# Performance work log

Measured on AMD Instinct MI355X. Metric: run time of the kernel, lower is better.

Reference implementation:

```python
import jax, jax.numpy as jnp
import numpy as np

N_NODES = 20000
N_EDGES = 320000
N_GRAPHS = 64
IN_DIM = 39
HID = 128
HEADS = 4
NUM_CONV = 3
PRED_HID = 32
N_TASKS = 1
NEG_SLOPE = 0.2


def setup_inputs() -> dict:
    key = jax.random.key(0)
    ks = jax.random.split(key, 16)
    node_feat = jax.random.normal(ks[0], (N_NODES, IN_DIM), dtype=jnp.float32)
    edge_index = jax.random.randint(ks[1], (2, N_EDGES), 0, N_NODES, dtype=jnp.int64)
    batch = jnp.sort(jax.random.randint(ks[2], (N_NODES,), 0, N_GRAPHS, dtype=jnp.int64))
    s = 0.05
    return {
        "node_feat": node_feat,
        "edge_index": edge_index,
        "batch": batch,
        "emb_W": jax.random.normal(ks[3], (IN_DIM, HID), dtype=jnp.float32) * s,
        "emb_b": jnp.zeros((HID,), dtype=jnp.float32),
        "lin_W": jax.random.normal(ks[4], (NUM_CONV, HID, HEADS * HID), dtype=jnp.float32) * s,
        "att_src": jax.random.normal(ks[5], (NUM_CONV, HEADS, HID), dtype=jnp.float32) * s,
        "att_dst": jax.random.normal(ks[6], (NUM_CONV, HEADS, HID), dtype=jnp.float32) * s,
        "conv_b": jnp.zeros((NUM_CONV, HID), dtype=jnp.float32),
        "fc_W": jax.random.normal(ks[7], (HID, PRED_HID), dtype=jnp.float32) * s,
        "fc_b": jnp.zeros((PRED_HID,), dtype=jnp.float32),
        "out_W": jax.random.normal(ks[8], (PRED_HID, N_TASKS), dtype=jnp.float32) * s,
        "out_b": jnp.zeros((N_TASKS,), dtype=jnp.float32),
    }


def _gat_layer(x, src, dst, W, a_src, a_dst, b):
    # PyG GATConv (concat=False): per-head projection, additive attention,
    # segment softmax over incoming edges of each target node, head-mean + bias.
    N = x.shape[0]
    h = (x @ W).reshape(N, HEADS, HID)            # [N, H, F]
    a_s = jnp.einsum('nhf,hf->nh', h, a_src)       # [N, H]
    a_d = jnp.einsum('nhf,hf->nh', h, a_dst)       # [N, H]
    e = jax.nn.leaky_relu(a_s[src] + a_d[dst], NEG_SLOPE)   # [E, H]
    e_max = jax.ops.segment_max(e, dst, num_segments=N)      # [N, H]
    e = jnp.exp(e - e_max[dst])
    denom = jax.ops.segment_sum(e, dst, num_segments=N)      # [N, H]
    alpha = e / denom[dst]                                    # [E, H]
    msg = h[src] * alpha[..., None]                           # [E, H, F]
    out = jax.ops.segment_sum(msg, dst, num_segments=N)      # [N, H, F]
    return out.mean(axis=1) + b                               # [N, F]


def reference(node_feat, edge_index, batch, emb_W, emb_b, lin_W, att_src, att_dst,
              conv_b, fc_W, fc_b, out_W, out_b):
    N = node_feat.shape[0]
    loops = jnp.arange(N, dtype=edge_index.dtype)
    src = jnp.concatenate([edge_index[0], loops])  # add_self_loops=True
    dst = jnp.concatenate([edge_index[1], loops])

    x = node_feat @ emb_W + emb_b
    for l in range(NUM_CONV):
        x = _gat_layer(x, src, dst, lin_W[l], att_src[l], att_dst[l], conv_b[l])

    # global_mean_pool
    sums = jax.ops.segment_sum(x, batch, num_segments=N_GRAPHS)              # [G, F]
    cnt = jax.ops.segment_sum(jnp.ones((N,), x.dtype), batch, num_segments=N_GRAPHS)
    g = sums / jnp.maximum(cnt, 1.0)[:, None]

    g = g @ fc_W + fc_b
    return g @ out_W + out_b
```

## Files before the change

### kernel.cpp

```cpp
#include <hip/hip_runtime.h>
#include <math.h>

#define N_NODES 20000
#define E0      320000
#define E_TOT   (E0 + N_NODES)
#define N_GRAPHS 64
#define IN_DIM  39
#define HID     128
#define HEADS   4
#define HHID    (HEADS * HID)
#define NUM_CONV 3
#define PRED_HID 32
#define NEG_SLOPE 0.2f

__device__ __forceinline__ int esrc(const int* __restrict__ ei, int e) {
    return e < E0 ? ei[e] : (e - E0);
}
__device__ __forceinline__ int edst(const int* __restrict__ ei, int e) {
    return e < E0 ? ei[E0 + e] : (e - E0);
}

__global__ void k_deg(const int* __restrict__ ei, int* __restrict__ deg) {
    int e = blockIdx.x * blockDim.x + threadIdx.x;
    if (e >= E_TOT) return;
    atomicAdd(&deg[edst(ei, e)], 1);
}

__global__ __launch_bounds__(1024) void k_scan(const int* __restrict__ deg,
                                               int* __restrict__ row_ptr,
                                               int* __restrict__ cursor) {
    __shared__ int part[1024];
    const int CHUNK = 20;
    int t = threadIdx.x;
    int base = t * CHUNK;
    int s = 0;
    for (int i = 0; i < CHUNK; i++) {
        int idx = base + i;
        if (idx < N_NODES) s += deg[idx];
    }
    part[t] = s;
    __syncthreads();
    for (int off = 1; off < 1024; off <<= 1) {
        int v = (t >= off) ? part[t - off] : 0;
        __syncthreads();
        part[t] += v;
        __syncthreads();
    }
    int run = part[t] - s;
    for (int i = 0; i < CHUNK; i++) {
        int idx = base + i;
        if (idx < N_NODES) {
            row_ptr[idx] = run;
            cursor[idx]  = run;
            run += deg[idx];
        }
    }
    if (t == 1023) row_ptr[N_NODES] = part[1023];
}

__global__ void k_scatter(const int* __restrict__ ei, int* __restrict__ cursor,
                          int* __restrict__ csr_src) {
    int e = blockIdx.x * blockDim.x + threadIdx.x;
    if (e >= E_TOT) return;
    int d = edst(ei, e);
    int pos = atomicAdd(&cursor[d], 1);
    csr_src[pos] = esrc(ei, e);
}

__global__ __launch_bounds__(128) void k_emb(const float* __restrict__ nf,
                                             const float* __restrict__ W,
                                             const float* __restrict__ b,
                                             float* __restrict__ x) {
    __shared__ float f[IN_DIM];
    int n = blockIdx.x, t = threadIdx.x;
    if (t < IN_DIM) f[t] = nf[(size_t)n * IN_DIM + t];
    __syncthreads();
    float acc = b[t];
#pragma unroll
    for (int k = 0; k < IN_DIM; k++) acc += f[k] * W[k * HID + t];
    x[(size_t)n * HID + t] = acc;
}

__global__ __launch_bounds__(128) void k_wsd(const float* __restrict__ lin_W,
                                             const float* __restrict__ attS,
                                             const float* __restrict__ attD,
                                             float* __restrict__ Wsd) {
    int l = blockIdx.x >> 3, j = blockIdx.x & 7, k = threadIdx.x;
    int h = j & 3;
    const float* Wl = lin_W + (size_t)l * HID * HHID;
    const float* av = ((j < 4) ? attS : attD) + ((size_t)l * HEADS + h) * HID;
    const float* wr = Wl + (size_t)k * HHID + h * HID;
    float dot = 0.f;
#pragma unroll 4
    for (int f = 0; f < HID; f++) dot += wr[f] * av[f];
    Wsd[(size_t)l * 8 * HID + j * HID + k] = dot;
}

__global__ __launch_bounds__(256) void k_attproj(const float* __restrict__ x,
                                                 const float* __restrict__ WsdL,
                                                 float* __restrict__ A8) {
    __shared__ float sW[8 * HID];
    for (int i = threadIdx.x; i < 8 * HID; i += 256) sW[i] = WsdL[i];
    __syncthreads();
    int wid = threadIdx.x >> 6, lane = threadIdx.x & 63;
    int n = blockIdx.x * 4 + wid;
    if (n >= N_NODES) return;
    float2 xv = *(const float2*)(x + (size_t)n * HID + lane * 2);
    float p[8];
#pragma unroll
    for (int j = 0; j < 8; j++) {
        float v = xv.x * sW[j * HID + lane * 2] + xv.y * sW[j * HID + lane * 2 + 1];
#pragma unroll
        for (int off = 32; off; off >>= 1) v += __shfl_xor(v, off, 64);
        p[j] = v;
    }
    if (lane == 0) {
        *(float4*)(A8 + (size_t)n * 8)     = make_float4(p[0], p[1], p[2], p[3]);
        *(float4*)(A8 + (size_t)n * 8 + 4) = make_float4(p[4], p[5], p[6], p[7]);
    }
}

__global__ __launch_bounds__(256) void k_aggr(const float* __restrict__ x,
                                              const int* __restrict__ row_ptr,
                                              const int* __restrict__ csr_src,
                                              const float* __restrict__ A8,
                                              float* __restrict__ agg) {
    int wid = threadIdx.x >> 6, lane = threadIdx.x & 63;
    int n = blockIdx.x * 4 + wid;
    if (n >= N_NODES) return;
    float4 vd = *(const float4*)(A8 + (size_t)n * 8 + 4);
    int beg = row_ptr[n], end = row_ptr[n + 1];
    float a0x = 0.f, a0y = 0.f, a1x = 0.f, a1y = 0.f;
    float a2x = 0.f, a2y = 0.f, a3x = 0.f, a3y = 0.f;
    float d0 = 0.f, d1 = 0.f, d2 = 0.f, d3 = 0.f;
    size_t lo = (size_t)(lane * 2);
    int eu = lane >> 2, eh = lane & 3;
    float vdh = (eh == 0) ? vd.x : (eh == 1) ? vd.y : (eh == 2) ? vd.z : vd.w;
    int i = beg;
    for (; i + 4 <= end; i += 4) {
        int s0 = csr_src[i];
        int s1 = csr_src[i + 1];
        int s2 = csr_src[i + 2];
        int s3 = csr_src[i + 3];
        float e = 0.f;
        if (lane < 16) {
            int su = (eu == 0) ? s0 : (eu == 1) ? s1 : (eu == 2) ? s2 : s3;
            float v = A8[(size_t)su * 8 + eh] + vdh;
            v = fmaxf(v, NEG_SLOPE * v);
            e = __expf(v);
        }
        float2 xv0 = *(const float2*)(x + (size_t)s0 * HID + lo);
        float2 xv1 = *(const float2*)(x + (size_t)s1 * HID + lo);
        float2 xv2 = *(const float2*)(x + (size_t)s2 * HID + lo);
        float2 xv3 = *(const float2*)(x + (size_t)s3 * HID + lo);
        float e00 = __shfl(e, 0, 64),  e01 = __shfl(e, 1, 64),  e02 = __shfl(e, 2, 64),  e03 = __shfl(e, 3, 64);
        float e10 = __shfl(e, 4, 64),  e11 = __shfl(e, 5, 64),  e12 = __shfl(e, 6, 64),  e13 = __shfl(e, 7, 64);
        float e20 = __shfl(e, 8, 64),  e21 = __shfl(e, 9, 64),  e22 = __shfl(e, 10, 64), e23 = __shfl(e, 11, 64);
        float e30 = __shfl(e, 12, 64), e31 = __shfl(e, 13, 64), e32 = __shfl(e, 14, 64), e33 = __shfl(e, 15, 64);
        a0x += e00 * xv0.x; a0y += e00 * xv0.y;
        a1x += e01 * xv0.x; a1y += e01 * xv0.y;
        a2x += e02 * xv0.x; a2y += e02 * xv0.y;
        a3x += e03 * xv0.x; a3y += e03 * xv0.y;
        d0 += e00; d1 += e01; d2 += e02; d3 += e03;
        a0x += e10 * xv1.x; a0y += e10 * xv1.y;
        a1x += e11 * xv1.x; a1y += e11 * xv1.y;
        a2x += e12 * xv1.x; a2y += e12 * xv1.y;
        a3x += e13 * xv1.x; a3y += e13 * xv1.y;
        d0 += e10; d1 += e11; d2 += e12; d3 += e13;
        a0x += e20 * xv2.x; a0y += e20 * xv2.y;
        a1x += e21 * xv2.x; a1y += e21 * xv2.y;
        a2x += e22 * xv2.x; a2y += e22 * xv2.y;
        a3x += e23 * xv2.x; a3y += e23 * xv2.y;
        d0 += e20; d1 += e21; d2 += e22; d3 += e23;
        a0x += e30 * xv3.x; a0y += e30 * xv3.y;
        a1x += e31 * xv3.x; a1y += e31 * xv3.y;
        a2x += e32 * xv3.x; a2y += e32 * xv3.y;
        a3x += e33 * xv3.x; a3y += e33 * xv3.y;
        d0 += e30; d1 += e31; d2 += e32; d3 += e33;
    }
    for (; i < end; i++) {
        int s0 = csr_src[i];
        float4 vs = *(const float4*)(A8 + (size_t)s0 * 8);
        float2 xv0 = *(const float2*)(x + (size_t)s0 * HID + lo);
        float v0 = vs.x + vd.x; v0 = fmaxf(v0, NEG_SLOPE * v0); float e0 = __expf(v0);
        float v1 = vs.y + vd.y; v1 = fmaxf(v1, NEG_SLOPE * v1); float e1 = __expf(v1);
        float v2 = vs.z + vd.z; v2 = fmaxf(v2, NEG_SLOPE * v2); float e2 = __expf(v2);
        float v3 = vs.w + vd.w; v3 = fmaxf(v3, NEG_SLOPE * v3); float e3 = __expf(v3);
        a0x += e0 * xv0.x; a0y += e0 * xv0.y;
        a1x += e1 * xv0.x; a1y += e1 * xv0.y;
        a2x += e2 * xv0.x; a2y += e2 * xv0.y;
        a3x += e3 * xv0.x; a3y += e3 * xv0.y;
        d0 += e0; d1 += e1; d2 += e2; d3 += e3;
    }
    float i0 = 1.f / d0, i1 = 1.f / d1, i2 = 1.f / d2, i3 = 1.f / d3;
    float* ag = agg + (size_t)n * HHID;
    *(float2*)(ag + 0 * HID + lo) = make_float2(a0x * i0, a0y * i0);
    *(float2*)(ag + 1 * HID + lo) = make_float2(a1x * i1, a1y * i1);
    *(float2*)(ag + 2 * HID + lo) = make_float2(a2x * i2, a2y * i2);
    *(float2*)(ag + 3 * HID + lo) = make_float2(a3x * i3, a3y * i3);
}

#define G2_BM 64
#define G2_KSPLIT 4
__global__ __launch_bounds__(256) void k_gemm2(const float* __restrict__ agg,
                                               const float* __restrict__ W,
                                               float* __restrict__ part, int M) {
    __shared__ float At[64][G2_BM];
    __shared__ float Bs[64][HID];
    int tid = threadIdx.x;
    int row0 = blockIdx.x * G2_BM;
    int ks = blockIdx.y;
    int ty = tid >> 4, tx = tid & 15;
    int r0 = ty * 4, c0 = tx * 4;
    float acc[4][8] = {};

#pragma unroll
    for (int kt = 0; kt < 2; kt++) {
        int kbase = ks * 128 + kt * 64;
        __syncthreads();
#pragma unroll
        for (int i = 0; i < 4; i++) {
            int idx = tid + i * 256;
            int r = idx >> 4;
            int c4 = idx & 15;
            int gr = row0 + r;
            float4 v = make_float4(0.f, 0.f, 0.f, 0.f);
            if (gr < M) v = *(const float4*)(agg + (size_t)gr * HHID + kbase + c4 * 4);
            int sw = (((r >> 2) ^ c4) << 2) + (r & 3);
            At[c4 * 4 + 0][sw] = v.x;
            At[c4 * 4 + 1][sw] = v.y;
            At[c4 * 4 + 2][sw] = v.z;
            At[c4 * 4 + 3][sw] = v.w;
        }
#pragma unroll
        for (int i = 0; i < 8; i++) {
            int idx = tid + i * 256;
            int kr = idx >> 5;
            int c4 = idx & 31;
            int kg = kbase + kr;
            int hd = kg >> 7, kk = kg & 127;
            *(float4*)(&Bs[kr][c4 * 4]) =
                *(const float4*)(W + (size_t)kk * HHID + hd * HID + c4 * 4);
        }
        __syncthreads();
#pragma unroll 4
        for (int k = 0; k < 64; k++) {
            float4 av = *(float4*)(&At[k][((ty ^ (k >> 2)) << 2)]);
            float4 b1 = *(float4*)(&Bs[k][c0]);
            float4 b2 = *(float4*)(&Bs[k][c0 + 64]);
            acc[0][0] += av.x * b1.x; acc[0][1] += av.x * b1.y; acc[0][2] += av.x * b1.z; acc[0][3] += av.x * b1.w;
            acc[0][4] += av.x * b2.x; acc[0][5] += av.x * b2.y; acc[0][6] += av.x * b2.z; acc[0][7] += av.x * b2.w;
            acc[1][0] += av.y * b1.x; acc[1][1] += av.y * b1.y; acc[1][2] += av.y * b1.z; acc[1][3] += av.y * b1.w;
            acc[1][4] += av.y * b2.x; acc[1][5] += av.y * b2.y; acc[1][6] += av.y * b2.z; acc[1][7] += av.y * b2.w;
            acc[2][0] += av.z * b1.x; acc[2][1] += av.z * b1.y; acc[2][2] += av.z * b1.z; acc[2][3] += av.z * b1.w;
            acc[2][4] += av.z * b2.x; acc[2][5] += av.z * b2.y; acc[2][6] += av.z * b2.z; acc[2][7] += av.z * b2.w;
            acc[3][0] += av.w * b1.x; acc[3][1] += av.w * b1.y; acc[3][2] += av.w * b1.z; acc[3][3] += av.w * b1.w;
            acc[3][4] += av.w * b2.x; acc[3][5] += av.w * b2.y; acc[3][6] += av.w * b2.z; acc[3][7] += av.w * b2.w;
        }
    }
    float* pb = part + (size_t)ks * M * HID;
#pragma unroll
    for (int i = 0; i < 4; i++) {
        int gr = row0 + r0 + i;
        if (gr < M) {
            *(float4*)(pb + (size_t)gr * HID + c0) =
                make_float4(acc[i][0], acc[i][1], acc[i][2], acc[i][3]);
            *(float4*)(pb + (size_t)gr * HID + c0 + 64) =
                make_float4(acc[i][4], acc[i][5], acc[i][6], acc[i][7]);
        }
    }
}

__global__ __launch_bounds__(256) void k_gfin(const float* __restrict__ part,
                                              const float* __restrict__ bias,
                                              const float* __restrict__ WsdL,
                                              float* __restrict__ xn,
                                              float* __restrict__ A8, int M) {
    __shared__ float sW[8 * HID];
    for (int i = threadIdx.x; i < 8 * HID; i += 256) sW[i] = WsdL[i];
    __syncthreads();
    int wid = threadIdx.x >> 6, lane = threadIdx.x & 63;
    int n = blockIdx.x * 4 + wid;
    if (n >= M) return;
    size_t off = (size_t)n * HID + lane * 2;
    size_t str = (size_t)M * HID;
    float2 p0 = *(const float2*)(part + off);
    float2 p1 = *(const float2*)(part + str + off);
    float2 p2 = *(const float2*)(part + 2 * str + off);
    float2 p3 = *(const float2*)(part + 3 * str + off);
    float2 bb = *(const float2*)(bias + lane * 2);
    float2 xv;
    xv.x = 0.25f * (p0.x + p1.x + p2.x + p3.x) + bb.x;
    xv.y = 0.25f * (p0.y + p1.y + p2.y + p3.y) + bb.y;
    *(float2*)(xn + off) = xv;
    float p[8];
#pragma unroll
    for (int j = 0; j < 8; j++) {
        float v = xv.x * sW[j * HID + lane * 2] + xv.y * sW[j * HID + lane * 2 + 1];
#pragma unroll
        for (int o = 32; o; o >>= 1) v += __shfl_xor(v, o, 64);
        p[j] = v;
    }
    if (lane == 0) {
        *(float4*)(A8 + (size_t)n * 8)     = make_float4(p[0], p[1], p[2], p[3]);
        *(float4*)(A8 + (size_t)n * 8 + 4) = make_float4(p[4], p[5], p[6], p[7]);
    }
}

#define POOL_NPB 64
__global__ __launch_bounds__(128) void k_pool(const float* __restrict__ x,
                                              const int* __restrict__ batch,
                                              float* __restrict__ g_sum,
                                              int* __restrict__ g_cnt) {
    int t = threadIdx.x;
    int n0 = blockIdx.x * POOL_NPB;
    int n1 = n0 + POOL_NPB; if (n1 > N_NODES) n1 = N_NODES;
    if (n0 >= n1) return;
    int cur = batch[n0];
    float acc = 0.f;
    int cnt = 0;
    for (int n = n0; n < n1; n++) {
        int b = batch[n];
        if (b != cur) {
            atomicAdd(&g_sum[cur * HID + t], acc);
            if (t == 0) atomicAdd(&g_cnt[cur], cnt);
            acc = 0.f; cnt = 0; cur = b;
        }
        acc += x[(size_t)n * HID + t];
        cnt++;
    }
    atomicAdd(&g_sum[cur * HID + t], acc);
    if (t == 0) atomicAdd(&g_cnt[cur], cnt);
}

__global__ __launch_bounds__(64) void k_head(const float* __restrict__ g_sum,
                                             const int* __restrict__ g_cnt,
                                             const float* __restrict__ fcW,
                                             const float* __restrict__ fcb,
                                             const float* __restrict__ outW,
                                             const float* __restrict__ outb,
                                             float* __restrict__ out) {
    int g = blockIdx.x, t = threadIdx.x;
    float inv = 1.f / fmaxf((float)g_cnt[g], 1.f);
    float val = 0.f;
    if (t < PRED_HID) {
        float dot = fcb[t];
        for (int f = 0; f < HID; f++)
            dot += (g_sum[g * HID + f] * inv) * fcW[f * PRED_HID + t];
        val = dot * outW[t];
    }
#pragma unroll
    for (int off = 32; off; off >>= 1) val += __shfl_xor(val, off, 64);
    if (t == 0) out[g] = val + outb[0];
}

extern "C" void kernel_launch(void* const* d_in, const int* in_sizes, int n_in,
                              void* d_out, int out_size, void* d_ws, size_t ws_size,
                              hipStream_t stream) {
    const float* node_feat = (const float*)d_in[0];
    const int*   edge_index = (const int*)d_in[1];
    const int*   batch     = (const int*)d_in[2];
    const float* emb_W     = (const float*)d_in[3];
    const float* emb_b     = (const float*)d_in[4];
    const float* lin_W     = (const float*)d_in[5];
    const float* att_src   = (const float*)d_in[6];
    const float* att_dst   = (const float*)d_in[7];
    const float* conv_b    = (const float*)d_in[8];
    const float* fc_W      = (const float*)d_in[9];
    const float* fc_b      = (const float*)d_in[10];
    const float* out_W     = (const float*)d_in[11];
    const float* out_b     = (const float*)d_in[12];
    float* out = (float*)d_out;

    char* p = (char*)d_ws;
    auto alloc = [&](size_t bytes) {
        void* r = (void*)p;
        p += (bytes + 255) & ~(size_t)255;
        return r;
    };
    float* x0      = (float*)alloc((size_t)N_NODES * HID * 4);
    float* x1      = (float*)alloc((size_t)N_NODES * HID * 4);
    float* agg     = (float*)alloc((size_t)N_NODES * HHID * 4);
    float* part    = (float*)alloc((size_t)G2_KSPLIT * N_NODES * HID * 4);
    float* A8      = (float*)alloc((size_t)N_NODES * 8 * 4);
    float* Wsd     = (float*)alloc((size_t)NUM_CONV * 8 * HID * 4);
    int*   deg     = (int*)alloc((size_t)(N_NODES + 1) * 4);
    int*   row_ptr = (int*)alloc((size_t)(N_NODES + 1) * 4);
    int*   cursor  = (int*)alloc((size_t)N_NODES * 4);
    int*   csr_src = (int*)alloc((size_t)E_TOT * 4);
    float* g_sum   = (float*)alloc((size_t)N_GRAPHS * HID * 4);
    int*   g_cnt   = (int*)alloc((size_t)N_GRAPHS * 4);

    const int EB = (E_TOT + 255) / 256;
    const int NB4 = (N_NODES + 3) / 4;

    hipMemsetAsync(deg, 0, (size_t)N_NODES * 4, stream);
    k_deg<<<EB, 256, 0, stream>>>(edge_index, deg);
    k_scan<<<1, 1024, 0, stream>>>(deg, row_ptr, cursor);
    k_scatter<<<EB, 256, 0, stream>>>(edge_index, cursor, csr_src);

    k_wsd<<<NUM_CONV * 8, 128, 0, stream>>>(lin_W, att_src, att_dst, Wsd);

    k_emb<<<N_NODES, 128, 0, stream>>>(node_feat, emb_W, emb_b, x0);
    k_attproj<<<NB4, 256, 0, stream>>>(x0, Wsd, A8);

    float* xin = x0;
    float* xout = x1;
    for (int l = 0; l < NUM_CONV; l++) {
        const float* Wl = lin_W + (size_t)l * HID * HHID;
        const float* bl = conv_b + (size_t)l * HID;
        int lnext = (l + 1 < NUM_CONV) ? l + 1 : NUM_CONV - 1;

        k_aggr<<<NB4, 256, 0, stream>>>(xin, row_ptr, csr_src, A8, agg);
        dim3 gg((N_NODES + G2_BM - 1) / G2_BM, G2_KSPLIT);
        k_gemm2<<<gg, 256, 0, stream>>>(agg, Wl, part, N_NODES);
        k_gfin<<<NB4, 256, 0, stream>>>(part, bl, Wsd + (size_t)lnext * 8 * HID,
                                        xout, A8, N_NODES);
        float* tmp = xin; xin = xout; xout = tmp;
    }

    hipMemsetAsync(g_sum, 0, (size_t)N_GRAPHS * HID * 4, stream);
    hipMemsetAsync(g_cnt, 0, (size_t)N_GRAPHS * 4, stream);
    k_pool<<<(N_NODES + POOL_NPB - 1) / POOL_NPB, 128, 0, stream>>>(xin, batch, g_sum, g_cnt);
    k_head<<<N_GRAPHS, 64, 0, stream>>>(g_sum, g_cnt, fc_W, fc_b,
                                        out_W, out_b, out);
}
```

Measured before the change: 410.9 us.

## Fuse whole GAT pipeline into one persistent cooperative kernel with grid syncs

Replaces the chain of separate kernel launches (CSR build, embedding, attention projection, per-layer aggregation, GEMM, finalize, pooling, head) with a single cooperative persistent kernel that separates phases using grid.sync(). The goal is to remove launch overhead and the inter-kernel gaps. The CSR scan becomes a multi-block hierarchical scan, and embedding is fused with the attention projection. In exchange, the grid is capped at the cooperative occupancy limit and every phase runs at that fixed parallelism, and the grid-wide barriers add cost. Heavy shared memory use at launch bounds of 3 blocks per CU may also limit occupancy for the gather-bound aggregation.

```diff
diff --git a/kernel.cpp b/kernel.cpp
--- a/kernel.cpp
+++ b/kernel.cpp
@@ -1,5 +1,8 @@
 #include <hip/hip_runtime.h>
+#include <hip/hip_cooperative_groups.h>
 #include <math.h>
+
+namespace cg = cooperative_groups;
 
 #define N_NODES 20000
 #define E0      320000
@@ -12,6 +15,18 @@
 #define NUM_CONV 3
 #define PRED_HID 32
 #define NEG_SLOPE 0.2f
+#define KSPLIT  4
+#define NTILES  ((N_NODES + 63) / 64)
+
+struct MegaParams {
+    const float* node_feat; const int* edge_index; const int* batch;
+    const float* emb_W; const float* emb_b; const float* lin_W;
+    const float* att_src; const float* att_dst; const float* conv_b;
+    const float* fc_W; const float* fc_b; const float* out_W; const float* out_b;
+    float* out;
+    float* x0; float* x1; float* agg; float* part; float* A8; float* Wsd;
+    int* deg; int* row_ptr; int* cursor; int* csr_src; int* bsum; int* bpre;
+};
 
 __device__ __forceinline__ int esrc(const int* __restrict__ ei, int e) {
     return e < E0 ? ei[e] : (e - E0);
@@ -19,409 +34,373 @@
 __device__ __forceinline__ int edst(const int* __restrict__ ei, int e) {
     return e < E0 ? ei[E0 + e] : (e - E0);
 }
-
-__global__ void k_deg(const int* __restrict__ ei, int* __restrict__ deg) {
-    int e = blockIdx.x * blockDim.x + threadIdx.x;
-    if (e >= E_TOT) return;
-    atomicAdd(&deg[edst(ei, e)], 1);
+__device__ __forceinline__ int lbound(const int* __restrict__ a, int n, int v) {
+    int lo = 0, hi = n;
+    while (lo < hi) { int m = (lo + hi) >> 1; if (a[m] < v) lo = m + 1; else hi = m; }
+    return lo;
 }
 
-__global__ __launch_bounds__(1024) void k_scan(const int* __restrict__ deg,
-                                               int* __restrict__ row_ptr,
-                                               int* __restrict__ cursor) {
-    __shared__ int part[1024];
-    const int CHUNK = 20;
-    int t = threadIdx.x;
-    int base = t * CHUNK;
-    int s = 0;
-    for (int i = 0; i < CHUNK; i++) {
-        int idx = base + i;
-        if (idx < N_NODES) s += deg[idx];
-    }
-    part[t] = s;
-    __syncthreads();
-    for (int off = 1; off < 1024; off <<= 1) {
-        int v = (t >= off) ? part[t - off] : 0;
+__global__ __launch_bounds__(256, 3) void k_mega(MegaParams P) {
+    cg::grid_group grid = cg::this_grid();
+    const int G = gridDim.x, b = blockIdx.x, tid = threadIdx.x;
+    const int gthread = b * 256 + tid, nthreads = G * 256;
+    const int wid = tid >> 6, lane = tid & 63;
+
+    __shared__ __align__(16) char smem_raw[49152];
+    int*   ib  = (int*)smem_raw;
+    float* fsh = (float*)smem_raw;
+    float* At  = (float*)smem_raw;
+    float* Bs  = (float*)(smem_raw + 16384);
+
+    for (int i = gthread; i < N_NODES; i += nthreads) P.deg[i] = 0;
+    for (int u = b; u < NUM_CONV * 8; u += G) {
+        int l = u >> 3, j = u & 7, h = j & 3;
+        if (tid < HID) {
+            const float* wr = P.lin_W + (size_t)l * HID * HHID + (size_t)tid * HHID + h * HID;
+            const float* av = ((j < 4) ? P.att_src : P.att_dst) + ((size_t)l * HEADS + h) * HID;
+            float dot = 0.f;
+            for (int f = 0; f < HID; f++) dot += wr[f] * av[f];
+            P.Wsd[(size_t)l * 8 * HID + j * HID + tid] = dot;
+        }
+    }
+    grid.sync();
+
+    for (int e = gthread; e < E_TOT; e += nthreads)
+        atomicAdd(&P.deg[edst(P.edge_index, e)], 1);
+    grid.sync();
+
+    const int C = (N_NODES + G - 1) / G;
+    const int nlo = b * C, nhi = (nlo + C < N_NODES) ? nlo + C : N_NODES;
+    {
+        int s = 0;
+        for (int i = nlo + tid; i < nhi; i += 256) s += P.deg[i];
+        ib[tid] = s; __syncthreads();
+        for (int off = 128; off; off >>= 1) { if (tid < off) ib[tid] += ib[tid + off]; __syncthreads(); }
+        if (tid == 0) P.bsum[b] = ib[0];
+    }
+    grid.sync();
+
+    if (b == 0) {
+        int per = (G + 255) / 256;
+        int vals[8]; int loc = 0;
+        for (int i2 = 0; i2 < per; i2++) {
+            int idx = tid * per + i2;
+            int v = (idx < G) ? P.bsum[idx] : 0;
+            vals[i2] = v; loc += v;
+        }
+        ib[tid] = loc; __syncthreads();
+        for (int off = 1; off < 256; off <<= 1) {
+            int v = (tid >= off) ? ib[tid - off] : 0;
+            __syncthreads(); ib[tid] += v; __syncthreads();
+        }
+        int run = ib[tid] - loc;
+        for (int i2 = 0; i2 < per; i2++) {
+            int idx = tid * per + i2;
+            if (idx < G) { P.bpre[idx] = run; run += vals[i2]; }
+        }
+        if (tid == 255) P.row_ptr[N_NODES] = ib[255];
+    }
+    grid.sync();
+
+    {
+        int cnt = nhi - nlo;
+        if (tid < cnt) ib[tid] = P.deg[nlo + tid];
         __syncthreads();
-        part[t] += v;
+        if (tid == 0) {
+            int run = P.bpre[b];
+            for (int i = 0; i < cnt; i++) { int d = ib[i]; ib[i] = run; run += d; }
+        }
         __syncthreads();
-    }
-    int run = part[t] - s;
-    for (int i = 0; i < CHUNK; i++) {
-        int idx = base + i;
-        if (idx < N_NODES) {
-            row_ptr[idx] = run;
-            cursor[idx]  = run;
-            run += deg[idx];
-        }
-    }
-    if (t == 1023) row_ptr[N_NODES] = part[1023];
-}
-
-__global__ void k_scatter(const int* __restrict__ ei, int* __restrict__ cursor,
-                          int* __restrict__ csr_src) {
-    int e = blockIdx.x * blockDim.x + threadIdx.x;
-    if (e >= E_TOT) return;
-    int d = edst(ei, e);
-    int pos = atomicAdd(&cursor[d], 1);
-    csr_src[pos] = esrc(ei, e);
-}
-
-__global__ __launch_bounds__(128) void k_emb(const float* __restrict__ nf,
-                                             const float* __restrict__ W,
-                                             const float* __restrict__ b,
-                                             float* __restrict__ x) {
-    __shared__ float f[IN_DIM];
-    int n = blockIdx.x, t = threadIdx.x;
-    if (t < IN_DIM) f[t] = nf[(size_t)n * IN_DIM + t];
-    __syncthreads();
-    float acc = b[t];
-#pragma unroll
-    for (int k = 0; k < IN_DIM; k++) acc += f[k] * W[k * HID + t];
-    x[(size_t)n * HID + t] = acc;
-}
-
-__global__ __launch_bounds__(128) void k_wsd(const float* __restrict__ lin_W,
-                                             const float* __restrict__ attS,
-                                             const float* __restrict__ attD,
-                                             float* __restrict__ Wsd) {
-    int l = blockIdx.x >> 3, j = blockIdx.x & 7, k = threadIdx.x;
-    int h = j & 3;
-    const float* Wl = lin_W + (size_t)l * HID * HHID;
-    const float* av = ((j < 4) ? attS : attD) + ((size_t)l * HEADS + h) * HID;
-    const float* wr = Wl + (size_t)k * HHID + h * HID;
-    float dot = 0.f;
+        if (tid < cnt) { P.row_ptr[nlo + tid] = ib[tid]; P.cursor[nlo + tid] = ib[tid]; }
+    }
+    grid.sync();
+
+    for (int e = gthread; e < E_TOT; e += nthreads) {
+        int d = edst(P.edge_index, e);
+        int pos = atomicAdd(&P.cursor[d], 1);
+        P.csr_src[pos] = esrc(P.edge_index, e);
+    }
+    for (int grp = b; grp < N_NODES / 4; grp += G) {
+        int n = grp * 4 + wid;
+        if (lane < IN_DIM) fsh[wid * 40 + lane] = P.node_feat[(size_t)n * IN_DIM + lane];
+        __syncthreads();
+        float2 acc = *(const float2*)(P.emb_b + lane * 2);
+#pragma unroll
+        for (int k = 0; k < IN_DIM; k++) {
+            float f = fsh[wid * 40 + k];
+            float2 w = *(const float2*)(P.emb_W + k * HID + lane * 2);
+            acc.x += f * w.x; acc.y += f * w.y;
+        }
+        *(float2*)(P.x0 + (size_t)n * HID + lane * 2) = acc;
+        float p[8];
+#pragma unroll
+        for (int j = 0; j < 8; j++) {
+            float2 w = *(const float2*)(P.Wsd + j * HID + lane * 2);
+            float v = acc.x * w.x + acc.y * w.y;
+#pragma unroll
+            for (int off = 32; off; off >>= 1) v += __shfl_xor(v, off, 64);
+            p[j] = v;
+        }
+        if (lane == 0) {
+            *(float4*)(P.A8 + (size_t)n * 8)     = make_float4(p[0], p[1], p[2], p[3]);
+            *(float4*)(P.A8 + (size_t)n * 8 + 4) = make_float4(p[4], p[5], p[6], p[7]);
+        }
+        __syncthreads();
+    }
+    grid.sync();
+
+    float* xin = P.x0;
+    float* xout = P.x1;
+    for (int l = 0; l < NUM_CONV; l++) {
+        const float* Wl = P.lin_W + (size_t)l * HID * HHID;
+        const float* bl = P.conv_b + (size_t)l * HID;
+        int lnext = (l + 1 < NUM_CONV) ? l + 1 : NUM_CONV - 1;
+        const float* WsdL = P.Wsd + (size_t)lnext * 8 * HID;
+
+        for (int grp = b; grp < N_NODES / 4; grp += G) {
+            int n = grp * 4 + wid;
+            float4 vd = *(const float4*)(P.A8 + (size_t)n * 8 + 4);
+            int beg = P.row_ptr[n], end = P.row_ptr[n + 1];
+            float a0x = 0.f, a0y = 0.f, a1x = 0.f, a1y = 0.f;
+            float a2x = 0.f, a2y = 0.f, a3x = 0.f, a3y = 0.f;
+            float d0 = 0.f, d1 = 0.f, d2 = 0.f, d3 = 0.f;
+            size_t lo2 = (size_t)(lane * 2);
+            int eu = lane >> 2, eh = lane & 3;
+            float vdh = (eh == 0) ? vd.x : (eh == 1) ? vd.y : (eh == 2) ? vd.z : vd.w;
+            int i = beg;
+            for (; i + 4 <= end; i += 4) {
+                int s0 = P.csr_src[i];
+                int s1 = P.csr_src[i + 1];
+                int s2 = P.csr_src[i + 2];
+                int s3 = P.csr_src[i + 3];
+                float e = 0.f;
+                if (lane < 16) {
+                    int su = (eu == 0) ? s0 : (eu == 1) ? s1 : (eu == 2) ? s2 : s3;
+                    float v = P.A8[(size_t)su * 8 + eh] + vdh;
+                    v = fmaxf(v, NEG_SLOPE * v);
+                    e = __expf(v);
+                }
+                float2 xv0 = *(const float2*)(xin + (size_t)s0 * HID + lo2);
+                float2 xv1 = *(const float2*)(xin + (size_t)s1 * HID + lo2);
+                float2 xv2 = *(const float2*)(xin + (size_t)s2 * HID + lo2);
+                float2 xv3 = *(const float2*)(xin + (size_t)s3 * HID + lo2);
+                float e00 = __shfl(e, 0, 64),  e01 = __shfl(e, 1, 64),  e02 = __shfl(e, 2, 64),  e03 = __shfl(e, 3, 64);
+                float e10 = __shfl(e, 4, 64),  e11 = __shfl(e, 5, 64),  e12 = __shfl(e, 6, 64),  e13 = __shfl(e, 7, 64);
+                float e20 = __shfl(e, 8, 64),  e21 = __shfl(e, 9, 64),  e22 = __shfl(e, 10, 64), e23 = __shfl(e, 11, 64);
+                float e30 = __shfl(e, 12, 64), e31 = __shfl(e, 13, 64), e32 = __shfl(e, 14, 64), e33 = __shfl(e, 15, 64);
+                a0x += e00 * xv0.x; a0y += e00 * xv0.y;
+                a1x += e01 * xv0.x; a1y += e01 * xv0.y;
+                a2x += e02 * xv0.x; a2y += e02 * xv0.y;
+                a3x += e03 * xv0.x; a3y += e03 * xv0.y;
+                d0 += e00; d1 += e01; d2 += e02; d3 += e03;
+                a0x += e10 * xv1.x; a0y += e10 * xv1.y;
+                a1x += e11 * xv1.x; a1y += e11 * xv1.y;
+                a2x += e12 * xv1.x; a2y += e12 * xv1.y;
+                a3x += e13 * xv1.x; a3y += e13 * xv1.y;
+                d0 += e10; d1 += e11; d2 += e12; d3 += e13;
+                a0x += e20 * xv2.x; a0y += e20 * xv2.y;
+                a1x += e21 * xv2.x; a1y += e21 * xv2.y;
+                a2x += e22 * xv2.x; a2y += e22 * xv2.y;
+                a3x += e23 * xv2.x; a3y += e23 * xv2.y;
+                d0 += e20; d1 += e21; d2 += e22; d3 += e23;
+                a0x += e30 * xv3.x; a0y += e30 * xv3.y;
+                a1x += e31 * xv3.x; a1y += e31 * xv3.y;
+                a2x += e32 * xv3.x; a2y += e32 * xv3.y;
+                a3x += e33 * xv3.x; a3y += e33 * xv3.y;
+                d0 += e30; d1 += e31; d2 += e32; d3 += e33;
+            }
+            for (; i < end; i++) {
+                int s0 = P.csr_src[i];
+                float4 vs = *(const float4*)(P.A8 + (size_t)s0 * 8);
+                float2 xv0 = *(const float2*)(xin + (size_t)s0 * HID + lo2);
+                float v0 = vs.x + vd.x; v0 = fmaxf(v0, NEG_SLOPE * v0); float e0 = __expf(v0);
+                float v1 = vs.y + vd.y; v1 = fmaxf(v1, NEG_SLOPE * v1); float e1 = __expf(v1);
+                float v2 = vs.z + vd.z; v2 = fmaxf(v2, NEG_SLOPE * v2); float e2 = __expf(v2);
+                float v3 = vs.w + vd.w; v3 = fmaxf(v3, NEG_SLOPE * v3); float e3 = __expf(v3);
+                a0x += e0 * xv0.x; a0y += e0 * xv0.y;
+                a1x += e1 * xv0.x; a1y += e1 * xv0.y;
+                a2x += e2 * xv0.x; a2y += e2 * xv0.y;
+                a3x += e3 * xv0.x; a3y += e3 * xv0.y;
+                d0 += e0; d1 += e1; d2 += e2; d3 += e3;
+            }
+            float i0 = 1.f / d0, i1 = 1.f / d1, i2 = 1.f / d2, i3 = 1.f / d3;
+            float* ag = P.agg + (size_t)n * HHID;
+            *(float2*)(ag + 0 * HID + lo2) = make_float2(a0x * i0, a0y * i0);
+            *(float2*)(ag + 1 * HID + lo2) = make_float2(a1x * i1, a1y * i1);
+            *(float2*)(ag + 2 * HID + lo2) = make_float2(a2x * i2, a2y * i2);
+            *(float2*)(ag + 3 * HID + lo2) = make_float2(a3x * i3, a3y * i3);
+        }
+        grid.sync();
+
+        {
+            int ty = tid >> 4, tx = tid & 15;
+            int r0 = ty * 4, c0 = tx * 4;
+            for (int u = b; u < NTILES * KSPLIT; u += G) {
+                int bm = u >> 2, ks = u & 3;
+                int row0 = bm * 64;
+                float acc[4][8] = {};
+#pragma unroll
+                for (int kt = 0; kt < 2; kt++) {
+                    int kbase = ks * 128 + kt * 64;
+                    __syncthreads();
+#pragma unroll
+                    for (int i = 0; i < 4; i++) {
+                        int idx = tid + i * 256;
+                        int r = idx >> 4, c4 = idx & 15;
+                        int gr = row0 + r;
+                        float4 v = make_float4(0.f, 0.f, 0.f, 0.f);
+                        if (gr < N_NODES) v = *(const float4*)(P.agg + (size_t)gr * HHID + kbase + c4 * 4);
+                        int sw = (((r >> 2) ^ c4) << 2) + (r & 3);
+                        At[(c4 * 4 + 0) * 64 + sw] = v.x;
+                        At[(c4 * 4 + 1) * 64 + sw] = v.y;
+                        At[(c4 * 4 + 2) * 64 + sw] = v.z;
+                        At[(c4 * 4 + 3) * 64 + sw] = v.w;
+                    }
+#pragma unroll
+                    for (int i = 0; i < 8; i++) {
+                        int idx = tid + i * 256;
+                        int kr = idx >> 5, c4 = idx & 31;
+                        int kg = kbase + kr;
+                        int hd = kg >> 7, kk = kg & 127;
+                        *(float4*)(Bs + kr * 128 + c4 * 4) =
+                            *(const float4*)(Wl + (size_t)kk * HHID + hd * HID + c4 * 4);
+                    }
+                    __syncthreads();
 #pragma unroll 4
-    for (int f = 0; f < HID; f++) dot += wr[f] * av[f];
-    Wsd[(size_t)l * 8 * HID + j * HID + k] = dot;
-}
-
-__global__ __launch_bounds__(256) void k_attproj(const float* __restrict__ x,
-                                                 const float* __restrict__ WsdL,
-                                                 float* __restrict__ A8) {
-    __shared__ float sW[8 * HID];
-    for (int i = threadIdx.x; i < 8 * HID; i += 256) sW[i] = WsdL[i];
-    __syncthreads();
-    int wid = threadIdx.x >> 6, lane = threadIdx.x & 63;
-    int n = blockIdx.x * 4 + wid;
-    if (n >= N_NODES) return;
-    float2 xv = *(const float2*)(x + (size_t)n * HID + lane * 2);
-    float p[8];
-#pragma unroll
-    for (int j = 0; j < 8; j++) {
-        float v = xv.x * sW[j * HID + lane * 2] + xv.y * sW[j * HID + lane * 2 + 1];
-#pragma unroll
-        for (int off = 32; off; off >>= 1) v += __shfl_xor(v, off, 64);
-        p[j] = v;
-    }
-    if (lane == 0) {
-        *(float4*)(A8 + (size_t)n * 8)     = make_float4(p[0], p[1], p[2], p[3]);
-        *(float4*)(A8 + (size_t)n * 8 + 4) = make_float4(p[4], p[5], p[6], p[7]);
-    }
-}
-
-__global__ __launch_bounds__(256) void k_aggr(const float* __restrict__ x,
-                                              const int* __restrict__ row_ptr,
-                                              const int* __restrict__ csr_src,
-                                              const float* __restrict__ A8,
-                                              float* __restrict__ agg) {
-    int wid = threadIdx.x >> 6, lane = threadIdx.x & 63;
-    int n = blockIdx.x * 4 + wid;
-    if (n >= N_NODES) return;
-    float4 vd = *(const float4*)(A8 + (size_t)n * 8 + 4);
-    int beg = row_ptr[n], end = row_ptr[n + 1];
-    float a0x = 0.f, a0y = 0.f, a1x = 0.f, a1y = 0.f;
-    float a2x = 0.f, a2y = 0.f, a3x = 0.f, a3y = 0.f;
-    float d0 = 0.f, d1 = 0.f, d2 = 0.f, d3 = 0.f;
-    size_t lo = (size_t)(lane * 2);
-    int eu = lane >> 2, eh = lane & 3;
-    float vdh = (eh == 0) ? vd.x : (eh == 1) ? vd.y : (eh == 2) ? vd.z : vd.w;
-    int i = beg;
-    for (; i + 4 <= end; i += 4) {
-        int s0 = csr_src[i];
-        int s1 = csr_src[i + 1];
-        int s2 = csr_src[i + 2];
-        int s3 = csr_src[i + 3];
-        float e = 0.f;
-        if (lane < 16) {
-            int su = (eu == 0) ? s0 : (eu == 1) ? s1 : (eu == 2) ? s2 : s3;
-            float v = A8[(size_t)su * 8 + eh] + vdh;
-            v = fmaxf(v, NEG_SLOPE * v);
-            e = __expf(v);
-        }
-        float2 xv0 = *(const float2*)(x + (size_t)s0 * HID + lo);
-        float2 xv1 = *(const float2*)(x + (size_t)s1 * HID + lo);
-        float2 xv2 = *(const float2*)(x + (size_t)s2 * HID + lo);
-        float2 xv3 = *(const float2*)(x + (size_t)s3 * HID + lo);
-        float e00 = __shfl(e, 0, 64),  e01 = __shfl(e, 1, 64),  e02 = __shfl(e, 2, 64),  e03 = __shfl(e, 3, 64);
-        float e10 = __shfl(e, 4, 64),  e11 = __shfl(e, 5, 64),  e12 = __shfl(e, 6, 64),  e13 = __shfl(e, 7, 64);
-        float e20 = __shfl(e, 8, 64),  e21 = __shfl(e, 9, 64),  e22 = __shfl(e, 10, 64), e23 = __shfl(e, 11, 64);
-        float e30 = __shfl(e, 12, 64), e31 = __shfl(e, 13, 64), e32 = __shfl(e, 14, 64), e33 = __shfl(e, 15, 64);
-        a0x += e00 * xv0.x; a0y += e00 * xv0.y;
-        a1x += e01 * xv0.x; a1y += e01 * xv0.y;
-        a2x += e02 * xv0.x; a2y += e02 * xv0.y;
-        a3x += e03 * xv0.x; a3y += e03 * xv0.y;
-        d0 += e00; d1 += e01; d2 += e02; d3 += e03;
-        a0x += e10 * xv1.x; a0y += e10 * xv1.y;
-        a1x += e11 * xv1.x; a1y += e11 * xv1.y;
-        a2x += e12 * xv1.x; a2y += e12 * xv1.y;
-        a3x += e13 * xv1.x; a3y += e13 * xv1.y;
-        d0 += e10; d1 += e11; d2 += e12; d3 += e13;
-        a0x += e20 * xv2.x; a0y += e20 * xv2.y;
-        a1x += e21 * xv2.x; a1y += e21 * xv2.y;
-        a2x += e22 * xv2.x; a2y += e22 * xv2.y;
-        a3x += e23 * xv2.x; a3y += e23 * xv2.y;
-        d0 += e20; d1 += e21; d2 += e22; d3 += e23;
-        a0x += e30 * xv3.x; a0y += e30 * xv3.y;
-        a1x += e31 * xv3.x; a1y += e31 * xv3.y;
-        a2x += e32 * xv3.x; a2y += e32 * xv3.y;
-        a3x += e33 * xv3.x; a3y += e33 * xv3.y;
-        d0 += e30; d1 += e31; d2 += e32; d3 += e33;
-    }
-    for (; i < end; i++) {
-        int s0 = csr_src[i];
-        float4 vs = *(const float4*)(A8 + (size_t)s0 * 8);
-        float2 xv0 = *(const float2*)(x + (size_t)s0 * HID + lo);
-        float v0 = vs.x + vd.x; v0 = fmaxf(v0, NEG_SLOPE * v0); float e0 = __expf(v0);
-        float v1 = vs.y + vd.y; v1 = fmaxf(v1, NEG_SLOPE * v1); float e1 = __expf(v1);
-        float v2 = vs.z + vd.z; v2 = fmaxf(v2, NEG_SLOPE * v2); float e2 = __expf(v2);
-        float v3 = vs.w + vd.w; v3 = fmaxf(v3, NEG_SLOPE * v3); float e3 = __expf(v3);
-        a0x += e0 * xv0.x; a0y += e0 * xv0.y;
-        a1x += e1 * xv0.x; a1y += e1 * xv0.y;
-        a2x += e2 * xv0.x; a2y += e2 * xv0.y;
-        a3x += e3 * xv0.x; a3y += e3 * xv0.y;
-        d0 += e0; d1 += e1; d2 += e2; d3 += e3;
-    }
-    float i0 = 1.f / d0, i1 = 1.f / d1, i2 = 1.f / d2, i3 = 1.f / d3;
-    float* ag = agg + (size_t)n * HHID;
-    *(float2*)(ag + 0 * HID + lo) = make_float2(a0x * i0, a0y * i0);
-    *(float2*)(ag + 1 * HID + lo) = make_float2(a1x * i1, a1y * i1);
-    *(float2*)(ag + 2 * HID + lo) = make_float2(a2x * i2, a2y * i2);
-    *(float2*)(ag + 3 * HID + lo) = make_float2(a3x * i3, a3y * i3);
-}
-
-#define G2_BM 64
-#define G2_KSPLIT 4
-__global__ __launch_bounds__(256) void k_gemm2(const float* __restrict__ agg,
-                                               const float* __restrict__ W,
-                                               float* __restrict__ part, int M) {
-    __shared__ float At[64][G2_BM];
-    __shared__ float Bs[64][HID];
-    int tid = threadIdx.x;
-    int row0 = blockIdx.x * G2_BM;
-    int ks = blockIdx.y;
-    int ty = tid >> 4, tx = tid & 15;
-    int r0 = ty * 4, c0 = tx * 4;
-    float acc[4][8] = {};
-
-#pragma unroll
-    for (int kt = 0; kt < 2; kt++) {
-        int kbase = ks * 128 + kt * 64;
+                    for (int k = 0; k < 64; k++) {
+                        float4 av = *(float4*)(At + k * 64 + ((ty ^ (k >> 2)) << 2));
+                        float4 b1 = *(float4*)(Bs + k * 128 + c0);
+                        float4 b2 = *(float4*)(Bs + k * 128 + c0 + 64);
+                        acc[0][0] += av.x * b1.x; acc[0][1] += av.x * b1.y; acc[0][2] += av.x * b1.z; acc[0][3] += av.x * b1.w;
+                        acc[0][4] += av.x * b2.x; acc[0][5] += av.x * b2.y; acc[0][6] += av.x * b2.z; acc[0][7] += av.x * b2.w;
+                        acc[1][0] += av.y * b1.x; acc[1][1] += av.y * b1.y; acc[1][2] += av.y * b1.z; acc[1][3] += av.y * b1.w;
+                        acc[1][4] += av.y * b2.x; acc[1][5] += av.y * b2.y; acc[1][6] += av.y * b2.z; acc[1][7] += av.y * b2.w;
+                        acc[2][0] += av.z * b1.x; acc[2][1] += av.z * b1.y; acc[2][2] += av.z * b1.z; acc[2][3] += av.z * b1.w;
+                        acc[2][4] += av.z * b2.x; acc[2][5] += av.z * b2.y; acc[2][6] += av.z * b2.z; acc[2][7] += av.z * b2.w;
+                        acc[3][0] += av.w * b1.x; acc[3][1] += av.w * b1.y; acc[3][2] += av.w * b1.z; acc[3][3] += av.w * b1.w;
+                        acc[3][4] += av.w * b2.x; acc[3][5] += av.w * b2.y; acc[3][6] += av.w * b2.z; acc[3][7] += av.w * b2.w;
+                    }
+                }
+                float* pb = P.part + (size_t)ks * N_NODES * HID;
+#pragma unroll
+                for (int i = 0; i < 4; i++) {
+                    int gr = row0 + r0 + i;
+                    if (gr < N_NODES) {
+                        *(float4*)(pb + (size_t)gr * HID + c0) =
+                            make_float4(acc[i][0], acc[i][1], acc[i][2], acc[i][3]);
+                        *(float4*)(pb + (size_t)gr * HID + c0 + 64) =
+                            make_float4(acc[i][4], acc[i][5], acc[i][6], acc[i][7]);
+                    }
+                }
+            }
+        }
+        grid.sync();
+
+        for (int grp = b; grp < N_NODES / 4; grp += G) {
+            int n = grp * 4 + wid;
+            size_t off = (size_t)n * HID + lane * 2;
+            size_t str = (size_t)N_NODES * HID;
+            float2 p0 = *(const float2*)(P.part + off);
+            float2 p1 = *(const float2*)(P.part + str + off);
+            float2 p2 = *(const float2*)(P.part + 2 * str + off);
+            float2 p3 = *(const float2*)(P.part + 3 * str + off);
+            float2 bb = *(const float2*)(bl + lane * 2);
+            float2 xv;
+            xv.x = 0.25f * (p0.x + p1.x + p2.x + p3.x) + bb.x;
+            xv.y = 0.25f * (p0.y + p1.y + p2.y + p3.y) + bb.y;
+            *(float2*)(xout + off) = xv;
+            float p[8];
+#pragma unroll
+            for (int j = 0; j < 8; j++) {
+                float2 w = *(const float2*)(WsdL + j * HID + lane * 2);
+                float v = xv.x * w.x + xv.y * w.y;
+#pragma unroll
+                for (int o = 32; o; o >>= 1) v += __shfl_xor(v, o, 64);
+                p[j] = v;
+            }
+            if (lane == 0) {
+                *(float4*)(P.A8 + (size_t)n * 8)     = make_float4(p[0], p[1], p[2], p[3]);
+                *(float4*)(P.A8 + (size_t)n * 8 + 4) = make_float4(p[4], p[5], p[6], p[7]);
+            }
+        }
+        grid.sync();
+
+        float* tmp = xin; xin = xout; xout = tmp;
+    }
+
+    if (b < N_GRAPHS) {
+        int g = b;
+        int start = lbound(P.batch, N_NODES, g);
+        int end   = lbound(P.batch, N_NODES, g + 1);
+        int t = tid & 127, half = tid >> 7;
+        float a = 0.f;
+        for (int n = start + half; n < end; n += 2) a += xin[(size_t)n * HID + t];
+        fsh[tid] = a; __syncthreads();
+        if (tid < HID) fsh[256 + tid] = (fsh[tid] + fsh[tid + 128]) / fmaxf((float)(end - start), 1.f);
         __syncthreads();
-#pragma unroll
-        for (int i = 0; i < 4; i++) {
-            int idx = tid + i * 256;
-            int r = idx >> 4;
-            int c4 = idx & 15;
-            int gr = row0 + r;
-            float4 v = make_float4(0.f, 0.f, 0.f, 0.f);
-            if (gr < M) v = *(const float4*)(agg + (size_t)gr * HHID + kbase + c4 * 4);
-            int sw = (((r >> 2) ^ c4) << 2) + (r & 3);
-            At[c4 * 4 + 0][sw] = v.x;
-            At[c4 * 4 + 1][sw] = v.y;
-            At[c4 * 4 + 2][sw] = v.z;
-            At[c4 * 4 + 3][sw] = v.w;
-        }
-#pragma unroll
-        for (int i = 0; i < 8; i++) {
-            int idx = tid + i * 256;
-            int kr = idx >> 5;
-            int c4 = idx & 31;
-            int kg = kbase + kr;
-            int hd = kg >> 7, kk = kg & 127;
-            *(float4*)(&Bs[kr][c4 * 4]) =
-                *(const float4*)(W + (size_t)kk * HHID + hd * HID + c4 * 4);
-        }
-        __syncthreads();
-#pragma unroll 4
-        for (int k = 0; k < 64; k++) {
-            float4 av = *(float4*)(&At[k][((ty ^ (k >> 2)) << 2)]);
-            float4 b1 = *(float4*)(&Bs[k][c0]);
-            float4 b2 = *(float4*)(&Bs[k][c0 + 64]);
-            acc[0][0] += av.x * b1.x; acc[0][1] += av.x * b1.y; acc[0][2] += av.x * b1.z; acc[0][3] += av.x * b1.w;
-            acc[0][4] += av.x * b2.x; acc[0][5] += av.x * b2.y; acc[0][6] += av.x * b2.z; acc[0][7] += av.x * b2.w;
-            acc[1][0] += av.y * b1.x; acc[1][1] += av.y * b1.y; acc[1][2] += av.y * b1.z; acc[1][3] += av.y * b1.w;
-            acc[1][4] += av.y * b2.x; acc[1][5] += av.y * b2.y; acc[1][6] += av.y * b2.z; acc[1][7] += av.y * b2.w;
-            acc[2][0] += av.z * b1.x; acc[2][1] += av.z * b1.y; acc[2][2] += av.z * b1.z; acc[2][3] += av.z * b1.w;
-            acc[2][4] += av.z * b2.x; acc[2][5] += av.z * b2.y; acc[2][6] += av.z * b2.z; acc[2][7] += av.z * b2.w;
-            acc[3][0] += av.w * b1.x; acc[3][1] += av.w * b1.y; acc[3][2] += av.w * b1.z; acc[3][3] += av.w * b1.w;
-            acc[3][4] += av.w * b2.x; acc[3][5] += av.w * b2.y; acc[3][6] += av.w * b2.z; acc[3][7] += av.w * b2.w;
-        }
-    }
-    float* pb = part + (size_t)ks * M * HID;
-#pragma unroll
-    for (int i = 0; i < 4; i++) {
-        int gr = row0 + r0 + i;
-        if (gr < M) {
-            *(float4*)(pb + (size_t)gr * HID + c0) =
-                make_float4(acc[i][0], acc[i][1], acc[i][2], acc[i][3]);
-            *(float4*)(pb + (size_t)gr * HID + c0 + 64) =
-                make_float4(acc[i][4], acc[i][5], acc[i][6], acc[i][7]);
-        }
-    }
-}
-
-__global__ __launch_bounds__(256) void k_gfin(const float* __restrict__ part,
-                                              const float* __restrict__ bias,
-                                              const float* __restrict__ WsdL,
-                                              float* __restrict__ xn,
-                                              float* __restrict__ A8, int M) {
-    __shared__ float sW[8 * HID];
-    for (int i = threadIdx.x; i < 8 * HID; i += 256) sW[i] = WsdL[i];
-    __syncthreads();
-    int wid = threadIdx.x >> 6, lane = threadIdx.x & 63;
-    int n = blockIdx.x * 4 + wid;
-    if (n >= M) return;
-    size_t off = (size_t)n * HID + lane * 2;
-    size_t str = (size_t)M * HID;
-    float2 p0 = *(const float2*)(part + off);
-    float2 p1 = *(const float2*)(part + str + off);
-    float2 p2 = *(const float2*)(part + 2 * str + off);
-    float2 p3 = *(const float2*)(part + 3 * str + off);
-    float2 bb = *(const float2*)(bias + lane * 2);
-    float2 xv;
-    xv.x = 0.25f * (p0.x + p1.x + p2.x + p3.x) + bb.x;
-    xv.y = 0.25f * (p0.y + p1.y + p2.y + p3.y) + bb.y;
-    *(float2*)(xn + off) = xv;
-    float p[8];
-#pragma unroll
-    for (int j = 0; j < 8; j++) {
-        float v = xv.x * sW[j * HID + lane * 2] + xv.y * sW[j * HID + lane * 2 + 1];
-#pragma unroll
-        for (int o = 32; o; o >>= 1) v += __shfl_xor(v, o, 64);
-        p[j] = v;
-    }
-    if (lane == 0) {
-        *(float4*)(A8 + (size_t)n * 8)     = make_float4(p[0], p[1], p[2], p[3]);
-        *(float4*)(A8 + (size_t)n * 8 + 4) = make_float4(p[4], p[5], p[6], p[7]);
-    }
-}
-
-#define POOL_NPB 64
-__global__ __launch_bounds__(128) void k_pool(const float* __restrict__ x,
-                                              const int* __restrict__ batch,
-                                              float* __restrict__ g_sum,
-                                              int* __restrict__ g_cnt) {
-    int t = threadIdx.x;
-    int n0 = blockIdx.x * POOL_NPB;
-    int n1 = n0 + POOL_NPB; if (n1 > N_NODES) n1 = N_NODES;
-    if (n0 >= n1) return;
-    int cur = batch[n0];
-    float acc = 0.f;
-    int cnt = 0;
-    for (int n = n0; n < n1; n++) {
-        int b = batch[n];
-        if (b != cur) {
-            atomicAdd(&g_sum[cur * HID + t], acc);
-            if (t == 0) atomicAdd(&g_cnt[cur], cnt);
-            acc = 0.f; cnt = 0; cur = b;
-        }
-        acc += x[(size_t)n * HID + t];
-        cnt++;
-    }
-    atomicAdd(&g_sum[cur * HID + t], acc);
-    if (t == 0) atomicAdd(&g_cnt[cur], cnt);
-}
-
-__global__ __launch_bounds__(64) void k_head(const float* __restrict__ g_sum,
-                                             const int* __restrict__ g_cnt,
-                                             const float* __restrict__ fcW,
-                                             const float* __restrict__ fcb,
-                                             const float* __restrict__ outW,
-                                             const float* __restrict__ outb,
-                                             float* __restrict__ out) {
-    int g = blockIdx.x, t = threadIdx.x;
-    float inv = 1.f / fmaxf((float)g_cnt[g], 1.f);
-    float val = 0.f;
-    if (t < PRED_HID) {
-        float dot = fcb[t];
-        for (int f = 0; f < HID; f++)
-            dot += (g_sum[g * HID + f] * inv) * fcW[f * PRED_HID + t];
-        val = dot * outW[t];
-    }
-#pragma unroll
-    for (int off = 32; off; off >>= 1) val += __shfl_xor(val, off, 64);
-    if (t == 0) out[g] = val + outb[0];
+        if (tid < 64) {
+            float val = 0.f;
+            if (tid < PRED_HID) {
+                float dot = P.fc_b[tid];
+                for (int f = 0; f < HID; f++) dot += fsh[256 + f] * P.fc_W[f * PRED_HID + tid];
+                val = dot * P.out_W[tid];
+            }
+#pragma unroll
+            for (int off = 16; off; off >>= 1) val += __shfl_down(val, off, 64);
+            if (tid == 0) P.out[g] = val + P.out_b[0];
+        }
+    }
 }
 
 extern "C" void kernel_launch(void* const* d_in, const int* in_sizes, int n_in,
                               void* d_out, int out_size, void* d_ws, size_t ws_size,
                               hipStream_t stream) {
-    const float* node_feat = (const float*)d_in[0];
-    const int*   edge_index = (const int*)d_in[1];
-    const int*   batch     = (const int*)d_in[2];
-    const float* emb_W     = (const float*)d_in[3];
-    const float* emb_b     = (const float*)d_in[4];
-    const float* lin_W     = (const float*)d_in[5];
-    const float* att_src   = (const float*)d_in[6];
-    const float* att_dst   = (const float*)d_in[7];
-    const float* conv_b    = (const float*)d_in[8];
-    const float* fc_W      = (const float*)d_in[9];
-    const float* fc_b      = (const float*)d_in[10];
-    const float* out_W     = (const float*)d_in[11];
-    const float* out_b     = (const float*)d_in[12];
-    float* out = (float*)d_out;
-
     char* p = (char*)d_ws;
     auto alloc = [&](size_t bytes) {
         void* r = (void*)p;
         p += (bytes + 255) & ~(size_t)255;
         return r;
     };
-    float* x0      = (float*)alloc((size_t)N_NODES * HID * 4);
-    float* x1      = (float*)alloc((size_t)N_NODES * HID * 4);
-    float* agg     = (float*)alloc((size_t)N_NODES * HHID * 4);
-    float* part    = (float*)alloc((size_t)G2_KSPLIT * N_NODES * HID * 4);
-    float* A8      = (float*)alloc((size_t)N_NODES * 8 * 4);
-    float* Wsd     = (float*)alloc((size_t)NUM_CONV * 8 * HID * 4);
-    int*   deg     = (int*)alloc((size_t)(N_NODES + 1) * 4);
-    int*   row_ptr = (int*)alloc((size_t)(N_NODES + 1) * 4);
-    int*   cursor  = (int*)alloc((size_t)N_NODES * 4);
-    int*   csr_src = (int*)alloc((size_t)E_TOT * 4);
-    float* g_sum   = (float*)alloc((size_t)N_GRAPHS * HID * 4);
-    int*   g_cnt   = (int*)alloc((size_t)N_GRAPHS * 4);
-
-    const int EB = (E_TOT + 255) / 256;
-    const int NB4 = (N_NODES + 3) / 4;
-
-    hipMemsetAsync(deg, 0, (size_t)N_NODES * 4, stream);
-    k_deg<<<EB, 256, 0, stream>>>(edge_index, deg);
-    k_scan<<<1, 1024, 0, stream>>>(deg, row_ptr, cursor);
-    k_scatter<<<EB, 256, 0, stream>>>(edge_index, cursor, csr_src);
-
-    k_wsd<<<NUM_CONV * 8, 128, 0, stream>>>(lin_W, att_src, att_dst, Wsd);
-
-    k_emb<<<N_NODES, 128, 0, stream>>>(node_feat, emb_W, emb_b, x0);
-    k_attproj<<<NB4, 256, 0, stream>>>(x0, Wsd, A8);
-
-    float* xin = x0;
-    float* xout = x1;
-    for (int l = 0; l < NUM_CONV; l++) {
-        const float* Wl = lin_W + (size_t)l * HID * HHID;
-        const float* bl = conv_b + (size_t)l * HID;
-        int lnext = (l + 1 < NUM_CONV) ? l + 1 : NUM_CONV - 1;
-
-        k_aggr<<<NB4, 256, 0, stream>>>(xin, row_ptr, csr_src, A8, agg);
-        dim3 gg((N_NODES + G2_BM - 1) / G2_BM, G2_KSPLIT);
-        k_gemm2<<<gg, 256, 0, stream>>>(agg, Wl, part, N_NODES);
-        k_gfin<<<NB4, 256, 0, stream>>>(part, bl, Wsd + (size_t)lnext * 8 * HID,
-                                        xout, A8, N_NODES);
-        float* tmp = xin; xin = xout; xout = tmp;
-    }
-
-    hipMemsetAsync(g_sum, 0, (size_t)N_GRAPHS * HID * 4, stream);
-    hipMemsetAsync(g_cnt, 0, (size_t)N_GRAPHS * 4, stream);
-    k_pool<<<(N_NODES + POOL_NPB - 1) / POOL_NPB, 128, 0, stream>>>(xin, batch, g_sum, g_cnt);
-    k_head<<<N_GRAPHS, 64, 0, stream>>>(g_sum, g_cnt, fc_W, fc_b,
-                                        out_W, out_b, out);
+    MegaParams mp;
+    mp.node_feat = (const float*)d_in[0];
+    mp.edge_index = (const int*)d_in[1];
+    mp.batch     = (const int*)d_in[2];
+    mp.emb_W     = (const float*)d_in[3];
+    mp.emb_b     = (const float*)d_in[4];
+    mp.lin_W     = (const float*)d_in[5];
+    mp.att_src   = (const float*)d_in[6];
+    mp.att_dst   = (const float*)d_in[7];
+    mp.conv_b    = (const float*)d_in[8];
+    mp.fc_W      = (const float*)d_in[9];
+    mp.fc_b      = (const float*)d_in[10];
+    mp.out_W     = (const float*)d_in[11];
+    mp.out_b     = (const float*)d_in[12];
+    mp.out       = (float*)d_out;
+
+    mp.x0      = (float*)alloc((size_t)N_NODES * HID * 4);
+    mp.x1      = (float*)alloc((size_t)N_NODES * HID * 4);
+    mp.agg     = (float*)alloc((size_t)N_NODES * HHID * 4);
+    mp.part    = (float*)alloc((size_t)KSPLIT * N_NODES * HID * 4);
+    mp.A8      = (float*)alloc((size_t)N_NODES * 8 * 4);
+    mp.Wsd     = (float*)alloc((size_t)NUM_CONV * 8 * HID * 4);
+    mp.deg     = (int*)alloc((size_t)(N_NODES + 1) * 4);
+    mp.row_ptr = (int*)alloc((size_t)(N_NODES + 1) * 4);
+    mp.cursor  = (int*)alloc((size_t)N_NODES * 4);
+    mp.csr_src = (int*)alloc((size_t)E_TOT * 4);
+    mp.bsum    = (int*)alloc((size_t)4096 * 4);
+    mp.bpre    = (int*)alloc((size_t)4096 * 4);
+
+    int dev = 0;
+    (void)hipGetDevice(&dev);
+    int cus = 256;
+    (void)hipDeviceGetAttribute(&cus, hipDeviceAttributeMultiprocessorCount, dev);
+    int maxB = 0;
+    if (hipOccupancyMaxActiveBlocksPerMultiprocessor(&maxB, (const void*)k_mega, 256, 0) != hipSuccess || maxB <= 0)
+        maxB = 2;
+    int grid = cus * maxB;
+    if (grid > 2048) grid = 2048;
+    if (grid < 128) grid = 128;
+
+    void* args[] = { (void*)&mp };
+    (void)hipLaunchCooperativeKernel((const void*)k_mega, dim3(grid), dim3(256), args, 0, stream);
 }
```

Measured after the change: 1.191 ms. 2.9x slower.
